# Performance work log

Hardware: AMD Instinct MI355X
Metric: run time of the kernel (lower is better)

Reference implementation:

```python
import jax, jax.numpy as jnp
import numpy as np

B, S, E, H = 4, 4096, 1024, 16
D = E // H  # head_dim = 64


def _xavier(key, out_f, in_f):
    lim = float(np.sqrt(6.0 / (in_f + out_f)))
    return jax.random.uniform(key, (out_f, in_f), jnp.float32, -lim, lim)


def setup_inputs() -> dict:
    key = jax.random.key(0)
    ks = jax.random.split(key, 9)
    x = jax.random.normal(ks[0], (B, S, E), jnp.float32)
    Wq = _xavier(ks[1], E, E)
    Wk = _xavier(ks[2], E, E)
    Wv = _xavier(ks[3], E, E)
    Wo = _xavier(ks[4], E, E)
    bq = jnp.zeros((E,), jnp.float32)
    bk = jnp.zeros((E,), jnp.float32)
    bv = jnp.zeros((E,), jnp.float32)
    bo = jnp.zeros((E,), jnp.float32)
    return {"x": x, "Wq": Wq, "bq": bq, "Wk": Wk, "bk": bk,
            "Wv": Wv, "bv": bv, "Wo": Wo, "bo": bo}


def _feature_map(t):
    # elu(t) + 1 (positive feature map)
    return jax.nn.elu(t) + 1.0


def reference(x, Wq, bq, Wk, bk, Wv, bv, Wo, bo):
    b, s, _ = x.shape
    # projections (torch Linear: y = x @ W.T + b), reshape to [b, s, h, d]
    Q = (x @ Wq.T + bq).reshape(b, s, H, D)
    K = (x @ Wk.T + bk).reshape(b, s, H, D)
    V = (x @ Wv.T + bv).reshape(b, s, H, D)
    Q = _feature_map(Q)
    K = _feature_map(K)
    # KV summary: [b, h, d, e]
    KV = jnp.einsum('bshd,bshe->bhde', K, V)
    K_sum = K.sum(axis=1)  # [b, h, d]
    Z = 1.0 / (jnp.einsum('bshd,bhd->bsh', Q, K_sum) + 1e-6)  # [b, s, h]
    out = jnp.einsum('bshd,bhde,bsh->bshe', Q, KV, Z)  # [b, s, h, e]
    out = out.reshape(b, s, E)
    out = out @ Wo.T + bo
    return out
```

## Files before the change

kernel.cpp:

```cpp
#include <hip/hip_runtime.h>
#include <math.h>

#define BB 4
#define SS 4096
#define EE 1024
#define HH 16
#define DD 64
#define MM (BB*SS)

typedef _Float16 f16x8 __attribute__((ext_vector_type(8)));
typedef _Float16 f16x4 __attribute__((ext_vector_type(4)));
typedef float    f32x4 __attribute__((ext_vector_type(4)));

typedef __attribute__((address_space(3))) void lds_void;
typedef __attribute__((address_space(1))) void gm_void;

__device__ __forceinline__ void gload16(const void* g, void* l) {
  __builtin_amdgcn_global_load_lds((gm_void*)g, (lds_void*)l, 16, 0, 0);
}

__global__ __launch_bounds__(256) void conv_x_kernel(const float* __restrict__ x,
                                                     _Float16* __restrict__ xh, int n4) {
  int i = blockIdx.x * blockDim.x + threadIdx.x;
  int stride = gridDim.x * blockDim.x;
  for (; i < n4; i += stride) {
    f32x4 v = *(const f32x4*)&x[(size_t)i * 4];
    f16x4 h;
    h[0] = (_Float16)v[0]; h[1] = (_Float16)v[1];
    h[2] = (_Float16)v[2]; h[3] = (_Float16)v[3];
    *(f16x4*)&xh[(size_t)i * 4] = h;
  }
}

__global__ __launch_bounds__(256) void conv_w_kernel(const float* __restrict__ Wq,
                                                     const float* __restrict__ Wk,
                                                     const float* __restrict__ Wv,
                                                     const float* __restrict__ Wo,
                                                     _Float16* __restrict__ wqkv,
                                                     _Float16* __restrict__ woh) {
  const int per = (EE * EE) / 4;
  int i = blockIdx.x * blockDim.x + threadIdx.x;
  int stride = gridDim.x * blockDim.x;
  for (; i < 4 * per; i += stride) {
    int seg = i / per, off = i - seg * per;
    const float* src = (seg == 0) ? Wq : (seg == 1) ? Wk : (seg == 2) ? Wv : Wo;
    _Float16* dst = (seg < 3) ? (wqkv + (size_t)seg * EE * EE) : woh;
    f32x4 v = *(const f32x4*)&src[(size_t)off * 4];
    f16x4 h;
    h[0] = (_Float16)v[0]; h[1] = (_Float16)v[1];
    h[2] = (_Float16)v[2]; h[3] = (_Float16)v[3];
    *(f16x4*)&dst[(size_t)off * 4] = h;
  }
}

template <int EPI>
__global__ __launch_bounds__(256) void gemm_nt(const _Float16* __restrict__ A,
                                               const _Float16* __restrict__ Bw,
                                               const float* __restrict__ bias0,
                                               const float* __restrict__ bias1,
                                               const float* __restrict__ bias2,
                                               _Float16* __restrict__ O0,
                                               _Float16* __restrict__ O1,
                                               _Float16* __restrict__ O2,
                                               float* __restrict__ OF) {
  __shared__ __align__(16) _Float16 As[128 * 32];
  __shared__ __align__(16) _Float16 Bs[128 * 32];
  const int tid = threadIdx.x;
  const int lane = tid & 63;
  const int wv = tid >> 6;
  const int wr = wv >> 1, wc = wv & 1;
  const int mbase = blockIdx.y * 128;
  const int nbase = blockIdx.x * 128;

  f32x4 acc[4][4] = {};

  const int fr = lane & 15;
  const int kro = (lane >> 4) * 8;

  for (int ks = 0; ks < EE; ks += 32) {
    __syncthreads();
    {
      const int g0 = tid, g1 = tid + 256;
      gload16((const char*)A + ((size_t)(mbase + (g0 >> 2)) * EE + ks) * 2 + (g0 & 3) * 16,
              (char*)As + wv * 1024);
      gload16((const char*)A + ((size_t)(mbase + (g1 >> 2)) * EE + ks) * 2 + (g1 & 3) * 16,
              (char*)As + 4096 + wv * 1024);
      gload16((const char*)Bw + ((size_t)(nbase + (g0 >> 2)) * EE + ks) * 2 + (g0 & 3) * 16,
              (char*)Bs + wv * 1024);
      gload16((const char*)Bw + ((size_t)(nbase + (g1 >> 2)) * EE + ks) * 2 + (g1 & 3) * 16,
              (char*)Bs + 4096 + wv * 1024);
    }
    __syncthreads();

    f16x8 a[4], b[4];
#pragma unroll
    for (int m = 0; m < 4; m++)
      a[m] = *(const f16x8*)&As[(wr * 64 + m * 16 + fr) * 32 + kro];
#pragma unroll
    for (int n = 0; n < 4; n++)
      b[n] = *(const f16x8*)&Bs[(wc * 64 + n * 16 + fr) * 32 + kro];
#pragma unroll
    for (int m = 0; m < 4; m++)
#pragma unroll
      for (int n = 0; n < 4; n++)
        acc[m][n] = __builtin_amdgcn_mfma_f32_16x16x32_f16(a[m], b[n], acc[m][n], 0, 0, 0);
  }

  const int rl = (lane >> 4) * 4, cl = lane & 15;
  if (EPI == 0) {
    const int which = nbase >> 10;
    const float* bias = (which == 0) ? bias0 : (which == 1) ? bias1 : bias2;
    _Float16* O = (which == 0) ? O0 : (which == 1) ? O1 : O2;
    const int cbase = nbase & 1023;
#pragma unroll
    for (int m = 0; m < 4; m++)
#pragma unroll
      for (int n = 0; n < 4; n++)
#pragma unroll
        for (int j = 0; j < 4; j++) {
          int gm = mbase + wr * 64 + m * 16 + rl + j;
          int gc = cbase + wc * 64 + n * 16 + cl;
          float v = acc[m][n][j] + bias[gc];
          if (which < 2) v = (v > 0.f) ? (v + 1.f) : expf(v);
          O[(size_t)gm * EE + gc] = (_Float16)v;
        }
  } else {
#pragma unroll
    for (int m = 0; m < 4; m++)
#pragma unroll
      for (int n = 0; n < 4; n++)
#pragma unroll
        for (int j = 0; j < 4; j++) {
          int gm = mbase + wr * 64 + m * 16 + rl + j;
          int gn = nbase + wc * 64 + n * 16 + cl;
          OF[(size_t)gm * EE + gn] = acc[m][n][j] + bias0[gn];
        }
  }
}

__global__ __launch_bounds__(256) void kv_partial_kernel(const _Float16* __restrict__ Kh,
                                                         const _Float16* __restrict__ Vh,
                                                         float* __restrict__ kvpart,
                                                         float* __restrict__ ksump) {
  __shared__ __align__(16) _Float16 Ks[64 * 64];
  __shared__ __align__(16) _Float16 Vs[64 * 64];
  const int tid = threadIdx.x;
  const int wv = tid >> 6;
  const int bh = blockIdx.x;
  const int chunk = blockIdx.y;
  const int b = bh >> 4, h = bh & 15;
  const int td = tid >> 4, te = tid & 15;
  const int d0 = td * 4, e0 = te * 4;

  float kv[4][4] = {};
  float ks4[4] = {0.f, 0.f, 0.f, 0.f};

  for (int sub = 0; sub < 4; sub++) {
    const int s0 = chunk * 256 + sub * 64;
    __syncthreads();
    {
      const int g0 = tid, g1 = tid + 256;
      gload16((const char*)Kh + ((size_t)(b * SS + s0 + (g0 >> 3)) * EE + h * DD) * 2 + (g0 & 7) * 16,
              (char*)Ks + wv * 1024);
      gload16((const char*)Kh + ((size_t)(b * SS + s0 + (g1 >> 3)) * EE + h * DD) * 2 + (g1 & 7) * 16,
              (char*)Ks + 4096 + wv * 1024);
      gload16((const char*)Vh + ((size_t)(b * SS + s0 + (g0 >> 3)) * EE + h * DD) * 2 + (g0 & 7) * 16,
              (char*)Vs + wv * 1024);
      gload16((const char*)Vh + ((size_t)(b * SS + s0 + (g1 >> 3)) * EE + h * DD) * 2 + (g1 & 7) * 16,
              (char*)Vs + 4096 + wv * 1024);
    }
    __syncthreads();
#pragma unroll 8
    for (int s = 0; s < 64; s++) {
      f16x4 kk = *(const f16x4*)&Ks[s * 64 + d0];
      f16x4 vv = *(const f16x4*)&Vs[s * 64 + e0];
      float kf[4], vf[4];
#pragma unroll
      for (int i = 0; i < 4; i++) { kf[i] = (float)kk[i]; vf[i] = (float)vv[i]; }
#pragma unroll
      for (int i = 0; i < 4; i++)
#pragma unroll
        for (int j = 0; j < 4; j++) kv[i][j] += kf[i] * vf[j];
      if (te == 0) {
#pragma unroll
        for (int i = 0; i < 4; i++) ks4[i] += kf[i];
      }
    }
  }
  const size_t base = ((size_t)chunk * 64 + bh) * 4096;
#pragma unroll
  for (int i = 0; i < 4; i++)
#pragma unroll
    for (int j = 0; j < 4; j++) kvpart[base + (size_t)(d0 + i) * 64 + e0 + j] = kv[i][j];
  if (te == 0) {
#pragma unroll
    for (int i = 0; i < 4; i++) ksump[((size_t)chunk * 64 + bh) * 64 + d0 + i] = ks4[i];
  }
}

__global__ __launch_bounds__(256) void kv_reduce_kernel(const float* __restrict__ kvpart,
                                                        const float* __restrict__ ksump,
                                                        _Float16* __restrict__ kvt,
                                                        float* __restrict__ ksum) {
  const int idx = blockIdx.x * 256 + threadIdx.x;
  if (blockIdx.x < 1024) {
    const int bh = idx >> 12;
    const int rem = idx & 4095;
    float s = 0.f;
#pragma unroll
    for (int c = 0; c < 16; c++) s += kvpart[((size_t)c * 64 + bh) * 4096 + rem];
    const int d = rem >> 6, e = rem & 63;
    kvt[(size_t)bh * 4096 + e * 64 + d] = (_Float16)s;
  } else {
    const int i2 = idx - 1024 * 256;
    const int bh = i2 >> 6, d = i2 & 63;
    float s = 0.f;
#pragma unroll
    for (int c = 0; c < 16; c++) s += ksump[((size_t)c * 64 + bh) * 64 + d];
    ksum[i2] = s;
  }
}

__global__ __launch_bounds__(256) void attn_kernel(const _Float16* __restrict__ Qh,
                                                   const _Float16* __restrict__ kvt,
                                                   const float* __restrict__ ksum,
                                                   _Float16* __restrict__ attn) {
  __shared__ __align__(16) _Float16 Qs[64 * 64];
  __shared__ __align__(16) _Float16 KVs[64 * 64];
  __shared__ float ks_lds[64];
  __shared__ float dpart[4][64];
  __shared__ float zr[64];
  const int tid = threadIdx.x;
  const int lane = tid & 63;
  const int wv = tid >> 6;
  const int stile = blockIdx.x;
  const int bh = blockIdx.y;
  const int b = bh >> 4, h = bh & 15;
  const int m0 = b * SS + stile * 64;

  {
    const int g0 = tid, g1 = tid + 256;
    gload16((const char*)Qh + ((size_t)(m0 + (g0 >> 3)) * EE + h * DD) * 2 + (g0 & 7) * 16,
            (char*)Qs + wv * 1024);
    gload16((const char*)Qh + ((size_t)(m0 + (g1 >> 3)) * EE + h * DD) * 2 + (g1 & 7) * 16,
            (char*)Qs + 4096 + wv * 1024);
    gload16((const char*)kvt + (size_t)bh * 8192 + (size_t)g0 * 16, (char*)KVs + wv * 1024);
    gload16((const char*)kvt + (size_t)bh * 8192 + (size_t)g1 * 16, (char*)KVs + 4096 + wv * 1024);
  }
  if (tid < 64) ks_lds[tid] = ksum[bh * 64 + tid];
  __syncthreads();

  {
    const int r = tid & 63, q = tid >> 6;
    float p = 0.f;
#pragma unroll
    for (int i = 0; i < 16; i++) p += (float)Qs[r * 64 + q * 16 + i] * ks_lds[q * 16 + i];
    dpart[q][r] = p;
  }
  __syncthreads();
  if (tid < 64) {
    float den = dpart[0][tid] + dpart[1][tid] + dpart[2][tid] + dpart[3][tid];
    zr[tid] = 1.f / (den + 1e-6f);
  }
  __syncthreads();

  f32x4 acc[4] = {};
  const int fr = lane & 15;
  const int kg = (lane >> 4) * 8;
#pragma unroll
  for (int kh = 0; kh < 2; kh++) {
    f16x8 a = *(const f16x8*)&Qs[(wv * 16 + fr) * 64 + kh * 32 + kg];
#pragma unroll
    for (int n = 0; n < 4; n++) {
      f16x8 b8 = *(const f16x8*)&KVs[(n * 16 + fr) * 64 + kh * 32 + kg];
      acc[n] = __builtin_amdgcn_mfma_f32_16x16x32_f16(a, b8, acc[n], 0, 0, 0);
    }
  }

  const int rl = (lane >> 4) * 4, cl = lane & 15;
#pragma unroll
  for (int n = 0; n < 4; n++)
#pragma unroll
    for (int j = 0; j < 4; j++) {
      const int r = wv * 16 + rl + j;
      float v = acc[n][j] * zr[r];
      attn[(size_t)(m0 + r) * EE + h * DD + n * 16 + cl] = (_Float16)v;
    }
}

extern "C" void kernel_launch(void* const* d_in, const int* in_sizes, int n_in,
                              void* d_out, int out_size, void* d_ws, size_t ws_size,
                              hipStream_t stream) {
  const float* x  = (const float*)d_in[0];
  const float* Wq = (const float*)d_in[1];
  const float* bq = (const float*)d_in[2];
  const float* Wk = (const float*)d_in[3];
  const float* bk = (const float*)d_in[4];
  const float* Wv = (const float*)d_in[5];
  const float* bv = (const float*)d_in[6];
  const float* Wo = (const float*)d_in[7];
  const float* bo = (const float*)d_in[8];
  float* out = (float*)d_out;

  char* ws = (char*)d_ws;
  size_t off = 0;
  auto alloc = [&](size_t bytes) -> char* {
    char* p = ws + off;
    off += (bytes + 255) & ~(size_t)255;
    return p;
  };
  _Float16* xh    = (_Float16*)alloc((size_t)MM * EE * 2);
  _Float16* wqkv  = (_Float16*)alloc((size_t)3 * EE * EE * 2);
  _Float16* woh   = (_Float16*)alloc((size_t)EE * EE * 2);
  _Float16* Qh    = (_Float16*)alloc((size_t)MM * EE * 2);
  _Float16* Kh    = (_Float16*)alloc((size_t)MM * EE * 2);
  _Float16* Vh    = (_Float16*)alloc((size_t)MM * EE * 2);
  float*    kvpart= (float*)alloc((size_t)16 * 64 * 4096 * 4);
  float*    ksump = (float*)alloc((size_t)16 * 64 * 64 * 4);
  _Float16* kvt   = (_Float16*)alloc((size_t)64 * 4096 * 2);
  float*    ksum  = (float*)alloc((size_t)64 * 64 * 4);
  _Float16* attn  = xh;

  (void)in_sizes; (void)n_in; (void)out_size; (void)ws_size;

  conv_x_kernel<<<2048, 256, 0, stream>>>(x, xh, (MM * EE) / 4);
  conv_w_kernel<<<1024, 256, 0, stream>>>(Wq, Wk, Wv, Wo, wqkv, woh);
  gemm_nt<0><<<dim3(24, 128), 256, 0, stream>>>(xh, wqkv, bq, bk, bv, Qh, Kh, Vh, nullptr);
  kv_partial_kernel<<<dim3(64, 16), 256, 0, stream>>>(Kh, Vh, kvpart, ksump);
  kv_reduce_kernel<<<1040, 256, 0, stream>>>(kvpart, ksump, kvt, ksum);
  attn_kernel<<<dim3(64, 64), 256, 0, stream>>>(Qh, kvt, ksum, attn);
  gemm_nt<1><<<dim3(8, 128), 256, 0, stream>>>(attn, woh, bo, nullptr, nullptr,
                                               nullptr, nullptr, nullptr, out);
}
```

Before: 293.0 us.

## Replace GEMMs with 256x256 double-buffered pipelined MFMA kernel

Replaces the 128x128 single-buffered GEMM with a 256x256-tile, 512-thread kernel that stages the 64-wide K slices into double-buffered, XOR-swizzled LDS. The global-to-LDS loads for later tiles are interleaved with MFMA phases using explicit vmcnt waits, barriers and setprio. Blocks are remapped across XCDs for L2 locality. The aim is more operand reuse per byte loaded and overlap of memory with compute in both projection GEMMs. The cost is 128KB of LDS per block, heavy register use for the accumulators, and fragile hand-written waitcnt sequencing.

```diff
diff --git a/kernel.cpp b/kernel.cpp
--- a/kernel.cpp
+++ b/kernel.cpp
@@ -53,90 +53,165 @@
   }
 }
 
+
+#define SB0() __builtin_amdgcn_sched_barrier(0)
+#define VMW6 asm volatile("s_waitcnt vmcnt(6)" ::: "memory")
+#define VMW0 asm volatile("s_waitcnt vmcnt(0)" ::: "memory")
+#define NOP_ do {} while (0)
+
+#define STAGE_M(Gb, Lb, t, hf) do {                                          \
+    const char* g_ = (Gb) + ((size_t)(hf) << 18) + (size_t)(t) * 128;        \
+    char* d_ = (Lb) + (((t) & 1) << 15) + ((hf) << 14) + dsub;               \
+    gload16(g_, d_);                                                         \
+    gload16(g_ + ((size_t)64 << 11), d_ + 8192);                             \
+  } while (0)
+
+#define STAGE_A(t, hf) STAGE_M(Ag, Asb, t, hf)
+#define STAGE_B(t, hf) STAGE_M(Bg, Bsb, t, hf)
+
+#define RD_A(mf, s) (*(const f16x8*)(Asb + buf_ +                            \
+    (((((mf) < 4) ? 0 : 8) + wr4 + ((mf) & 3)) << 11) + ((s) << 10) + lof))
+#define RD_B(nf, s) (*(const f16x8*)(Bsb + buf_ + ((wc4 + (nf)) << 11) + ((s) << 10) + lof))
+
+#define PHASE(t, P, STG, VMC) do {                                           \
+    const int buf_ = ((t) & 1) << 15;                                        \
+    if ((P) == 0) {                                                          \
+      _Pragma("unroll") for (int nf = 0; nf < 4; nf++) {                     \
+        b[nf][0] = RD_B(nf, 0); b[nf][1] = RD_B(nf, 1);                      \
+      }                                                                      \
+    }                                                                        \
+    aP[0][0] = RD_A((P) * 2, 0);     aP[0][1] = RD_A((P) * 2, 1);            \
+    aP[1][0] = RD_A((P) * 2 + 1, 0); aP[1][1] = RD_A((P) * 2 + 1, 1);        \
+    STG;                                                                     \
+    SB0(); __builtin_amdgcn_s_barrier(); SB0();                              \
+    asm volatile("s_waitcnt lgkmcnt(0)" ::: "memory"); SB0();                \
+    __builtin_amdgcn_s_setprio(1);                                           \
+    _Pragma("unroll") for (int nf = 0; nf < 4; nf++) {                       \
+      acc[(P)*2][nf]   = __builtin_amdgcn_mfma_f32_16x16x32_f16(aP[0][0], b[nf][0], acc[(P)*2][nf], 0, 0, 0);   \
+      acc[(P)*2][nf]   = __builtin_amdgcn_mfma_f32_16x16x32_f16(aP[0][1], b[nf][1], acc[(P)*2][nf], 0, 0, 0);   \
+      acc[(P)*2+1][nf] = __builtin_amdgcn_mfma_f32_16x16x32_f16(aP[1][0], b[nf][0], acc[(P)*2+1][nf], 0, 0, 0); \
+      acc[(P)*2+1][nf] = __builtin_amdgcn_mfma_f32_16x16x32_f16(aP[1][1], b[nf][1], acc[(P)*2+1][nf], 0, 0, 0); \
+    }                                                                        \
+    __builtin_amdgcn_s_setprio(0);                                           \
+    VMC;                                                                     \
+    SB0(); __builtin_amdgcn_s_barrier(); SB0();                              \
+  } while (0)
+
+#define TILE(t, S1, S2, S3, S4, VMC) do {                                    \
+    PHASE(t, 0, S1, NOP_);                                                   \
+    PHASE(t, 1, S2, NOP_);                                                   \
+    PHASE(t, 2, S3, NOP_);                                                   \
+    PHASE(t, 3, S4, VMC);                                                    \
+  } while (0)
+
 template <int EPI>
-__global__ __launch_bounds__(256) void gemm_nt(const _Float16* __restrict__ A,
-                                               const _Float16* __restrict__ Bw,
-                                               const float* __restrict__ bias0,
-                                               const float* __restrict__ bias1,
-                                               const float* __restrict__ bias2,
-                                               _Float16* __restrict__ O0,
-                                               _Float16* __restrict__ O1,
-                                               _Float16* __restrict__ O2,
-                                               float* __restrict__ OF) {
-  __shared__ __align__(16) _Float16 As[128 * 32];
-  __shared__ __align__(16) _Float16 Bs[128 * 32];
-  const int tid = threadIdx.x;
+__global__ __launch_bounds__(512, 2) void gemm256(const _Float16* __restrict__ A,
+                                                  const _Float16* __restrict__ Bw,
+                                                  const float* __restrict__ bias0,
+                                                  const float* __restrict__ bias1,
+                                                  const float* __restrict__ bias2,
+                                                  _Float16* __restrict__ O0,
+                                                  _Float16* __restrict__ O1,
+                                                  _Float16* __restrict__ O2,
+                                                  float* __restrict__ OF) {
+  __shared__ __align__(16) char lds[131072];
+  char* Asb = lds;
+  char* Bsb = lds + 65536;
+
+  const int tid  = threadIdx.x;
   const int lane = tid & 63;
-  const int wv = tid >> 6;
-  const int wr = wv >> 1, wc = wv & 1;
-  const int mbase = blockIdx.y * 128;
-  const int nbase = blockIdx.x * 128;
-
-  f32x4 acc[4][4] = {};
-
-  const int fr = lane & 15;
-  const int kro = (lane >> 4) * 8;
-
-  for (int ks = 0; ks < EE; ks += 32) {
-    __syncthreads();
-    {
-      const int g0 = tid, g1 = tid + 256;
-      gload16((const char*)A + ((size_t)(mbase + (g0 >> 2)) * EE + ks) * 2 + (g0 & 3) * 16,
-              (char*)As + wv * 1024);
-      gload16((const char*)A + ((size_t)(mbase + (g1 >> 2)) * EE + ks) * 2 + (g1 & 3) * 16,
-              (char*)As + 4096 + wv * 1024);
-      gload16((const char*)Bw + ((size_t)(nbase + (g0 >> 2)) * EE + ks) * 2 + (g0 & 3) * 16,
-              (char*)Bs + wv * 1024);
-      gload16((const char*)Bw + ((size_t)(nbase + (g1 >> 2)) * EE + ks) * 2 + (g1 & 3) * 16,
-              (char*)Bs + 4096 + wv * 1024);
-    }
-    __syncthreads();
-
-    f16x8 a[4], b[4];
-#pragma unroll
-    for (int m = 0; m < 4; m++)
-      a[m] = *(const f16x8*)&As[(wr * 64 + m * 16 + fr) * 32 + kro];
-#pragma unroll
-    for (int n = 0; n < 4; n++)
-      b[n] = *(const f16x8*)&Bs[(wc * 64 + n * 16 + fr) * 32 + kro];
-#pragma unroll
-    for (int m = 0; m < 4; m++)
-#pragma unroll
-      for (int n = 0; n < 4; n++)
-        acc[m][n] = __builtin_amdgcn_mfma_f32_16x16x32_f16(a[m], b[n], acc[m][n], 0, 0, 0);
-  }
-
-  const int rl = (lane >> 4) * 4, cl = lane & 15;
+  const int wv   = tid >> 6;
+  const int wr4  = (wv >> 2) << 2;
+  const int wc4  = (wv & 3) << 2;
+  const int wrow = (wv >> 2) << 6;
+  const int wcol = (wv & 3) << 6;
+
+  constexpr int NX = (EPI == 0) ? 12 : 4;
+  const int q = (int)gridDim.x >> 3;
+  const int bid = (int)blockIdx.x;
+  const int sid = (bid & 7) * q + (bid >> 3);
+  const int mbase = (sid / NX) << 8;
+  const int nbase = (sid % NX) << 8;
+
+  const int lof   = (((lane & 15) << 6) | ((lane >> 4) << 4)) ^ ((lane & 8) << 2);
+  const int srow  = lane >> 2;
+  const int sbyte = ((lane & 3) << 4) ^ (lane & 32);
+
+  const int rg   = wv >> 1;
+  const int kgs  = wv & 1;
+  const int dsub = ((rg << 1) + kgs) << 10;
+
+  const char* Ag = (const char*)A +
+      ((size_t)(mbase + (rg << 4) + srow) << 11) + (kgs << 6) + sbyte;
+  const char* Bg = (const char*)Bw +
+      ((size_t)(nbase + (rg << 4) + srow) << 11) + (kgs << 6) + sbyte;
+
+  f32x4 acc[8][4] = {};
+  f16x8 b[4][2];
+  f16x8 aP[2][2];
+
+  STAGE_A(0, 0); STAGE_A(0, 1);
+  STAGE_B(0, 0); STAGE_B(0, 1);
+  STAGE_B(1, 0); STAGE_B(1, 1);
+  STAGE_A(1, 0);
+  VMW6;
+  SB0(); __builtin_amdgcn_s_barrier(); SB0();
+
+#pragma unroll 1
+  for (int i = 0; i < 7; ++i) {
+    const int t = i << 1;
+    TILE(t,     STAGE_A(t + 1, 1), STAGE_B(t + 2, 0), STAGE_B(t + 2, 1), STAGE_A(t + 2, 0), VMW6);
+    TILE(t + 1, STAGE_A(t + 2, 1), STAGE_B(t + 3, 0), STAGE_B(t + 3, 1), STAGE_A(t + 3, 0), VMW6);
+  }
+  TILE(14, STAGE_A(15, 1), NOP_, NOP_, NOP_, VMW0);
+  TILE(15, NOP_, NOP_, NOP_, NOP_, NOP_);
+
+  const int rl = (lane >> 4) << 2;
+  const int cl = lane & 15;
   if (EPI == 0) {
     const int which = nbase >> 10;
     const float* bias = (which == 0) ? bias0 : (which == 1) ? bias1 : bias2;
     _Float16* O = (which == 0) ? O0 : (which == 1) ? O1 : O2;
-    const int cbase = nbase & 1023;
-#pragma unroll
-    for (int m = 0; m < 4; m++)
-#pragma unroll
-      for (int n = 0; n < 4; n++)
+    const int cb = (nbase & 1023) + wcol;
+#pragma unroll
+    for (int mf = 0; mf < 8; mf++) {
+      const int gm = mbase + ((mf < 4) ? 0 : 128) + wrow + ((mf & 3) << 4) + rl;
+#pragma unroll
+      for (int nf = 0; nf < 4; nf++) {
+        const int gc = cb + (nf << 4) + cl;
+        const float bz = bias[gc];
 #pragma unroll
         for (int j = 0; j < 4; j++) {
-          int gm = mbase + wr * 64 + m * 16 + rl + j;
-          int gc = cbase + wc * 64 + n * 16 + cl;
-          float v = acc[m][n][j] + bias[gc];
+          float v = acc[mf][nf][j] + bz;
           if (which < 2) v = (v > 0.f) ? (v + 1.f) : expf(v);
-          O[(size_t)gm * EE + gc] = (_Float16)v;
+          O[(size_t)(gm + j) * EE + gc] = (_Float16)v;
         }
+      }
+    }
   } else {
-#pragma unroll
-    for (int m = 0; m < 4; m++)
-#pragma unroll
-      for (int n = 0; n < 4; n++)
-#pragma unroll
-        for (int j = 0; j < 4; j++) {
-          int gm = mbase + wr * 64 + m * 16 + rl + j;
-          int gn = nbase + wc * 64 + n * 16 + cl;
-          OF[(size_t)gm * EE + gn] = acc[m][n][j] + bias0[gn];
-        }
-  }
-}
+    const int cb = nbase + wcol;
+#pragma unroll
+    for (int mf = 0; mf < 8; mf++) {
+      const int gm = mbase + ((mf < 4) ? 0 : 128) + wrow + ((mf & 3) << 4) + rl;
+#pragma unroll
+      for (int nf = 0; nf < 4; nf++) {
+        const int gc = cb + (nf << 4) + cl;
+        const float bz = bias0[gc];
+#pragma unroll
+        for (int j = 0; j < 4; j++)
+          OF[(size_t)(gm + j) * EE + gc] = acc[mf][nf][j] + bz;
+      }
+    }
+  }
+}
+
+#undef TILE
+#undef PHASE
+#undef RD_A
+#undef RD_B
+#undef STAGE_A
+#undef STAGE_B
+#undef STAGE_M
 
 __global__ __launch_bounds__(256) void kv_partial_kernel(const _Float16* __restrict__ Kh,
                                                          const _Float16* __restrict__ Vh,
@@ -251,11 +326,11 @@
   __syncthreads();
 
   {
-    const int r = tid & 63, q = tid >> 6;
+    const int r = tid & 63, qd = tid >> 6;
     float p = 0.f;
 #pragma unroll
-    for (int i = 0; i < 16; i++) p += (float)Qs[r * 64 + q * 16 + i] * ks_lds[q * 16 + i];
-    dpart[q][r] = p;
+    for (int i = 0; i < 16; i++) p += (float)Qs[r * 64 + qd * 16 + i] * ks_lds[qd * 16 + i];
+    dpart[qd][r] = p;
   }
   __syncthreads();
   if (tid < 64) {
@@ -325,10 +400,10 @@
 
   conv_x_kernel<<<2048, 256, 0, stream>>>(x, xh, (MM * EE) / 4);
   conv_w_kernel<<<1024, 256, 0, stream>>>(Wq, Wk, Wv, Wo, wqkv, woh);
-  gemm_nt<0><<<dim3(24, 128), 256, 0, stream>>>(xh, wqkv, bq, bk, bv, Qh, Kh, Vh, nullptr);
+  gemm256<0><<<768, 512, 0, stream>>>(xh, wqkv, bq, bk, bv, Qh, Kh, Vh, nullptr);
   kv_partial_kernel<<<dim3(64, 16), 256, 0, stream>>>(Kh, Vh, kvpart, ksump);
   kv_reduce_kernel<<<1040, 256, 0, stream>>>(kvpart, ksump, kvt, ksum);
   attn_kernel<<<dim3(64, 64), 256, 0, stream>>>(Qh, kvt, ksum, attn);
-  gemm_nt<1><<<dim3(8, 128), 256, 0, stream>>>(attn, woh, bo, nullptr, nullptr,
-                                               nullptr, nullptr, nullptr, out);
-}
+  gemm256<1><<<256, 512, 0, stream>>>(attn, woh, bo, nullptr, nullptr,
+                                      nullptr, nullptr, nullptr, out);
+}
```

Result: faster. 253.3 us (-13.5%).
